# Kernel tuning notes

Hardware: AMD Instinct MI355X
Metric: run time of the kernel (lower is better)

The kernel has to match this reference:

```python
import jax, jax.numpy as jnp
import numpy as np
from jax.scipy.special import logsumexp

SINKHORN_ITERS = 10


def _fix_coupling_sinkhorn(lc, lp1, lp2, iterations=SINKHORN_ITERS):
    # lc: [Z,S], lp1: [Z], lp2: [S]
    for _ in range(iterations):
        lc = lc + lp1[:, None] - logsumexp(lc, axis=1, keepdims=True)
        lc = lc + lp2[None, :] - logsumexp(lc, axis=0, keepdims=True)
    return lc


def _fix_coupling_rejection(lc, lp1, lp2):
    fixed_p1 = lc + lp1[:, None] - logsumexp(lc, axis=1, keepdims=True)
    approx_lp2 = logsumexp(fixed_p1, axis=0)
    accept = lp2 - approx_lp2
    accept = accept - jnp.max(accept)
    acc_s2_given_s1 = jax.nn.log_softmax(fixed_p1, axis=-1) + accept[None, :]
    log_keep = logsumexp(acc_s2_given_s1, axis=-1)
    certainly_keep = jnp.exp(log_keep) >= 1.0
    resample = jnp.where(
        certainly_keep, -jnp.inf,
        jnp.log1p(-jnp.where(certainly_keep, 0.0, jnp.exp(log_keep))))
    compensation = resample[:, None] + lp2[None, :]
    return lp1[:, None] + jnp.logaddexp(acc_s2_given_s1, compensation)


def setup_inputs() -> dict:
    key = jax.random.key(0)
    ks = jax.random.split(key, 8)
    B, S, Z, H1, H2 = 64, 512, 1024, 512, 256
    return {
        "s_logits": jax.random.normal(ks[0], (B, S), jnp.float32),
        "W1": jax.random.normal(ks[1], (S, H1), jnp.float32) / np.sqrt(S),
        "b1": jnp.zeros((H1,), jnp.float32),
        "W2": jax.random.normal(ks[2], (H1, H2), jnp.float32) / np.sqrt(H1),
        "b2": jnp.zeros((H2,), jnp.float32),
        "Wout": jax.random.normal(ks[3], (H2, Z, S), jnp.float32) / np.sqrt(H2),
        "bout": jnp.zeros((Z, S), jnp.float32),
        "prior": jax.random.normal(ks[4], (Z,), jnp.float32) * 0.05,
    }


def reference(s_logits, W1, b1, W2, b2, Wout, bout, prior):
    z_logits = jax.nn.log_softmax(prior)  # [Z]

    def get_joint(sl):  # sl: [S]
        v = jax.nn.softmax(sl)
        v = jax.nn.sigmoid(v @ W1 + b1)
        v = jax.nn.sigmoid(v @ W2 + b2)
        log_joint = jnp.einsum('h,hzs->zs', v, Wout) + bout  # [Z,S]
        log_joint = _fix_coupling_sinkhorn(log_joint, z_logits, sl)
        return _fix_coupling_rejection(log_joint, z_logits, sl)

    return jax.vmap(get_joint)(s_logits)  # [B,Z,S]
```

## Files before the change

### kernel.cpp

```cpp
#include <hip/hip_runtime.h>
#include <math.h>

#define Bn 64
#define Sn 512
#define Zn 1024
#define H1n 512
#define H2n 256
#define ZSn (Zn*Sn)

#define OFF_LP1  0
#define OFF_VT   1024
#define OFF_V    17408
#define OFF_W    50176
#define OFF_R    82944
#define OFF_PM   148480
#define OFF_PS   672768
#define OFF_VB   1200128
#define OFF_KB   1310720
#define NEED_BF16_BYTES ((size_t)OFF_KB*4 + (size_t)Bn*ZSn*2)

#define NINF (-__builtin_inff())

typedef __attribute__((ext_vector_type(8))) short          s16x8;
typedef __attribute__((ext_vector_type(8))) unsigned short u16x8;
typedef __attribute__((ext_vector_type(4))) float          f32x4;

__device__ __forceinline__ float wred_max(float x){
#pragma unroll
  for (int o=32;o;o>>=1) x = fmaxf(x, __shfl_xor(x, o, 64));
  return x;
}
__device__ __forceinline__ float wred_sum(float x){
#pragma unroll
  for (int o=32;o;o>>=1) x += __shfl_xor(x, o, 64);
  return x;
}
__device__ __forceinline__ float lae(float a, float c){
  float m = fmaxf(a,c), n = fminf(a,c);
  return m + log1pf(__expf(n-m));
}
__device__ __forceinline__ float toF(float v){ return v; }
__device__ __forceinline__ float toF(unsigned short v){ return __uint_as_float(((unsigned int)v)<<16); }
__device__ __forceinline__ unsigned short bf16rne(float f){
  unsigned int u = __float_as_uint(f);
  return (unsigned short)((u + 0x7fffu + ((u>>16)&1u)) >> 16);
}
__device__ __forceinline__ unsigned int pack2(float a, float b){
  unsigned int ua = __float_as_uint(a), ub = __float_as_uint(b);
  ua = (ua + 0x7fffu + ((ua>>16)&1u)) >> 16;
  ub = (ub + 0x7fffu + ((ub>>16)&1u)) & 0xffff0000u;
  return ua | ub;
}

__global__ __launch_bounds__(512) void prep_kernel(const float* __restrict__ prior,
                                                   float* __restrict__ ws){
  __shared__ float red[8];
  int t = threadIdx.x;
  float x0 = prior[t], x1 = prior[t+512];
  float m = wred_max(fmaxf(x0,x1));
  if ((t&63)==0) red[t>>6] = m;
  __syncthreads();
  float M = red[0];
#pragma unroll
  for (int i=1;i<8;i++) M = fmaxf(M, red[i]);
  float e = __expf(x0-M)+__expf(x1-M);
  e = wred_sum(e);
  __syncthreads();
  if ((t&63)==0) red[t>>6] = e;
  __syncthreads();
  float T = 0.f;
#pragma unroll
  for (int i=0;i<8;i++) T += red[i];
  float lse = M + logf(T);
  ws[OFF_LP1 + t]       = x0 - lse;
  ws[OFF_LP1 + t + 512] = x1 - lse;
}

__global__ __launch_bounds__(512) void mlp_kernel(const float* __restrict__ sl,
    const float* __restrict__ W1, const float* __restrict__ b1,
    const float* __restrict__ W2, const float* __restrict__ b2,
    float* __restrict__ ws, int wbf){
  __shared__ float p[Sn];
  __shared__ float h1s[H1n];
  __shared__ float red[8];
  int b = blockIdx.x, t = threadIdx.x;
  float x = sl[b*Sn + t];
  float m = wred_max(x);
  if ((t&63)==0) red[t>>6] = m;
  __syncthreads();
  float M = red[0];
#pragma unroll
  for (int i=1;i<8;i++) M = fmaxf(M, red[i]);
  float e = __expf(x-M);
  float es = wred_sum(e);
  __syncthreads();
  if ((t&63)==0) red[t>>6] = es;
  __syncthreads();
  float T = 0.f;
#pragma unroll
  for (int i=0;i<8;i++) T += red[i];
  p[t] = e / T;
  __syncthreads();
  float acc = b1[t];
#pragma unroll 8
  for (int s=0;s<Sn;s++) acc = fmaf(p[s], W1[s*H1n + t], acc);
  h1s[t] = 1.f/(1.f+__expf(-acc));
  __syncthreads();
  if (t < H2n){
    float a2 = b2[t];
#pragma unroll 8
    for (int s=0;s<H1n;s++) a2 = fmaf(h1s[s], W2[s*H2n + t], a2);
    float vv = 1.f/(1.f+__expf(-a2));
    ws[OFF_VT + t*Bn + b] = vv;
    if (wbf) ((unsigned short*)(ws + OFF_VB))[b*H2n + t] = bf16rne(vv);
  }
}

template<int BF>
__global__ __launch_bounds__(256,1) void gemm_kernel(const float* __restrict__ Wout,
    const float* __restrict__ bout, const float* __restrict__ ws,
    float* __restrict__ Kf, unsigned int* __restrict__ Kb){
  int zh = blockIdx.x*256 + threadIdx.x;
  const float* __restrict__ VT = ws + OFF_VT;
  float2 acc[Bn];
#pragma unroll
  for (int b=0;b<Bn;b++){ acc[b].x = 0.f; acc[b].y = 0.f; }
  const float2* Wp = (const float2*)Wout;
#pragma unroll 2
  for (int h=0; h<H2n; h++){
    float2 wv = Wp[(size_t)h*(ZSn/2) + zh];
    const float* vh = VT + (h<<6);
#pragma unroll
    for (int b=0;b<Bn;b++){
      acc[b].x = fmaf(vh[b], wv.x, acc[b].x);
      acc[b].y = fmaf(vh[b], wv.y, acc[b].y);
    }
  }
  float2 bb = ((const float2*)bout)[zh];
#pragma unroll
  for (int b=0;b<Bn;b++){
    float ax = acc[b].x + bb.x, ay = acc[b].y + bb.y;
    if (BF){
      Kb[(size_t)b*(ZSn/2) + zh] = pack2(ax, ay);
    } else {
      float2 o; o.x = ax; o.y = ay;
      ((float2*)Kf)[(size_t)b*(ZSn/2) + zh] = o;
    }
  }
}

__global__ __launch_bounds__(256,3) void gemm_mfma(const float* __restrict__ Wout,
    const float* __restrict__ bout, const float* __restrict__ ws,
    unsigned short* __restrict__ Kb){
  __shared__ unsigned short Vsh[64*264];
  __shared__ float Bsh[32*65];
  int t = threadIdx.x;
  int zs0 = blockIdx.x * 64;

  {
    const unsigned short* vsrc = (const unsigned short*)(ws + OFF_VB);
    int vrow = t >> 2, vq = t & 3;
#pragma unroll
    for (int i=0;i<8;i++)
      *(u16x8*)&Vsh[vrow*264 + vq*64 + i*8] = *(const u16x8*)&vsrc[vrow*256 + vq*64 + i*8];
  }

  int w  = t >> 6;
  int l  = t & 63;
  int q  = l & 15;
  int kg = l >> 4;
  int sh = t >> 3, sf = t & 7;

  float bo = bout[zs0 + (w<<4) + q];

  f32x4 acc[4] = {{0.f,0.f,0.f,0.f},{0.f,0.f,0.f,0.f},{0.f,0.f,0.f,0.f},{0.f,0.f,0.f,0.f}};

  const float4* src = (const float4*)(Wout + (size_t)sh * ZSn + zs0);
  float4 ra = src[sf], rb = src[sf+8];

  for (int ks=0; ks<8; ks++){
    __syncthreads();
    {
      float* drow = &Bsh[sh*65 + (sf<<2)];
      drow[0]=ra.x; drow[1]=ra.y; drow[2]=ra.z; drow[3]=ra.w;
      drow[32]=rb.x; drow[33]=rb.y; drow[34]=rb.z; drow[35]=rb.w;
    }
    if (ks < 7){
      const float4* s2 = (const float4*)(Wout + (size_t)((ks+1)*32 + sh) * ZSn + zs0);
      ra = s2[sf]; rb = s2[sf+8];
    }
    __syncthreads();
    float bf[8];
#pragma unroll
    for (int j=0;j<8;j++) bf[j] = Bsh[(kg*8+j)*65 + (w<<4) + q];
    unsigned int pk[4];
#pragma unroll
    for (int j=0;j<4;j++)
      asm("v_cvt_pk_bf16_f32 %0, %1, %2" : "=v"(pk[j]) : "v"(bf[2*j]), "v"(bf[2*j+1]));
    union { unsigned int u[4]; s16x8 v; } bu;
    bu.u[0]=pk[0]; bu.u[1]=pk[1]; bu.u[2]=pk[2]; bu.u[3]=pk[3];
#pragma unroll
    for (int mt=0; mt<4; mt++){
      s16x8 af = *(const s16x8*)&Vsh[(mt*16 + q)*264 + ks*32 + kg*8];
      acc[mt] = __builtin_amdgcn_mfma_f32_16x16x32_bf16(af, bu.v, acc[mt], 0, 0, 0);
    }
  }
#pragma unroll
  for (int mt=0; mt<4; mt++){
#pragma unroll
    for (int r=0; r<4; r++){
      int b = mt*16 + kg*4 + r;
      Kb[(size_t)b*ZSn + zs0 + (w<<4) + q] = bf16rne(acc[mt][r] + bo);
    }
  }
}

template<typename KT>
__global__ __launch_bounds__(512) void iter_fused(const KT* __restrict__ Kg,
    float* __restrict__ ws, const float* __restrict__ sl, int iter, int mode){
  __shared__ KT Ksh[64*512];
  __shared__ float vsh[512];
  __shared__ float ush[64];
  __shared__ float lsh[64];
  int t = threadIdx.x;
  int b = blockIdx.x >> 4, c = blockIdx.x & 15;
  const float4* s4 = (const float4*)(Kg + ((size_t)((b<<10) + (c<<6)) << 9));
  float4* d4 = (float4*)Ksh;
  constexpr int NV = (int)sizeof(KT)*4;
#pragma unroll
  for (int i=0;i<NV;i++) d4[i*512 + t] = s4[i*512 + t];
  if (t < 64) lsh[t] = ws[OFF_LP1 + (c<<6) + t];
  float v_s;
  if (iter == 0) v_s = 0.f;
  else {
    float M = NINF, S = 0.f;
#pragma unroll
    for (int cc=0; cc<16; cc++){
      float m = ws[OFF_PM + ((b*16+cc)<<9) + t];
      float p = ws[OFF_PS + ((b*16+cc)<<9) + t];
      float nm = fmaxf(M, m);
      S = S*__expf(M-nm) + p*__expf(m-nm);
      M = nm;
    }
    v_s = sl[(b<<9) + t] - (M + logf(S));
  }
  vsh[t] = v_s;
  if (mode) ws[OFF_V + (b<<9) + t] = v_s;
  __syncthreads();
  int l = t & 63, w = t >> 6;
  float vr[8];
#pragma unroll
  for (int j=0;j<8;j++) vr[j] = vsh[(l<<3)+j];
#pragma unroll
  for (int rr=0; rr<8; rr++){
    int row = (w<<3) + rr;
    float x[8];
    if constexpr (sizeof(KT)==2){
      u16x8 kv = *(const u16x8*)&Ksh[(row<<9) + (l<<3)];
#pragma unroll
      for (int j=0;j<8;j++) x[j] = toF((unsigned short)kv[j]) + vr[j];
    } else {
      const float4* kp = (const float4*)&Ksh[(row<<9) + (l<<3)];
      float4 k0 = kp[0], k1 = kp[1];
      x[0]=k0.x+vr[0]; x[1]=k0.y+vr[1]; x[2]=k0.z+vr[2]; x[3]=k0.w+vr[3];
      x[4]=k1.x+vr[4]; x[5]=k1.y+vr[5]; x[6]=k1.z+vr[6]; x[7]=k1.w+vr[7];
    }
    float m = NINF;
#pragma unroll
    for (int j=0;j<8;j++) m = fmaxf(m, x[j]);
    m = wred_max(m);
    float s = 0.f;
#pragma unroll
    for (int j=0;j<8;j++) s += __expf(x[j]-m);
    s = wred_sum(s);
    float L = m + logf(s);
    if (l == 0){
      ush[row] = lsh[row] - L;
      if (mode) ws[OFF_R + (b<<10) + (c<<6) + row] = L;
    }
  }
  __syncthreads();
  float M0 = NINF, S0 = 0.f, M1 = NINF, S1 = 0.f;
#pragma unroll 8
  for (int i=0;i<32;i++){
    float xa = toF(Ksh[(i<<9) + t]) + ush[i];
    float na = fmaxf(M0, xa);
    S0 = S0*__expf(M0-na) + __expf(xa-na);
    M0 = na;
    float xb = toF(Ksh[((i+32)<<9) + t]) + ush[i+32];
    float nb = fmaxf(M1, xb);
    S1 = S1*__expf(M1-nb) + __expf(xb-nb);
    M1 = nb;
  }
  float M = fmaxf(M0, M1);
  float S = S0*__expf(M0-M) + S1*__expf(M1-M);
  ws[OFF_PM + ((b*16+c)<<9) + t] = M;
  ws[OFF_PS + ((b*16+c)<<9) + t] = S;
}

__global__ __launch_bounds__(512) void wker(float* __restrict__ ws, const float* __restrict__ sl){
  __shared__ float red[8];
  int b = blockIdx.x, s = threadIdx.x;
  float M = NINF, S = 0.f;
#pragma unroll
  for (int cc=0; cc<16; cc++){
    float m = ws[OFF_PM + ((b*16+cc)<<9) + s];
    float p = ws[OFF_PS + ((b*16+cc)<<9) + s];
    float nm = fmaxf(M, m);
    S = S*__expf(M-nm) + p*__expf(m-nm);
    M = nm;
  }
  float L = M + logf(S);
  float v = ws[OFF_V + (b<<9) + s];
  float araw = sl[(b<<9)+s] - v - L;
  float mm = wred_max(araw);
  if ((s&63)==0) red[s>>6] = mm;
  __syncthreads();
  float amax = red[0];
#pragma unroll
  for (int i=1;i<8;i++) amax = fmaxf(amax, red[i]);
  ws[OFF_W + (b<<9) + s] = v + araw - amax;
}

template<typename KT>
__global__ __launch_bounds__(512) void final_fused(const KT* __restrict__ Kg,
    float* __restrict__ out, const float* __restrict__ ws, const float* __restrict__ sl){
  int t = threadIdx.x, l = t & 63, wv = t >> 6;
  int row = blockIdx.x*8 + wv;
  int b = row >> 10, z = row & (Zn-1);
  const KT* Kr = Kg + ((size_t)row << 9);
  const float* wr = ws + OFF_W + (b << 9);
  const float* pr = sl + (b << 9);
  float r  = ws[OFF_R + row];
  float l1 = ws[OFF_LP1 + z];
  float ww[8], pp[8], kk[8];
  {
    const float4* wp = (const float4*)(wr + (l<<3));
    float4 w0 = wp[0], w1 = wp[1];
    ww[0]=w0.x; ww[1]=w0.y; ww[2]=w0.z; ww[3]=w0.w;
    ww[4]=w1.x; ww[5]=w1.y; ww[6]=w1.z; ww[7]=w1.w;
    const float4* pt = (const float4*)(pr + (l<<3));
    float4 p0 = pt[0], p1 = pt[1];
    pp[0]=p0.x; pp[1]=p0.y; pp[2]=p0.z; pp[3]=p0.w;
    pp[4]=p1.x; pp[5]=p1.y; pp[6]=p1.z; pp[7]=p1.w;
  }
  if constexpr (sizeof(KT)==2){
    u16x8 kv = *(const u16x8*)&Kr[l<<3];
#pragma unroll
    for (int j=0;j<8;j++) kk[j] = toF((unsigned short)kv[j]);
  } else {
    const float4* kp = (const float4*)&Kr[l<<3];
    float4 k0 = kp[0], k1 = kp[1];
    kk[0]=k0.x; kk[1]=k0.y; kk[2]=k0.z; kk[3]=k0.w;
    kk[4]=k1.x; kk[5]=k1.y; kk[6]=k1.z; kk[7]=k1.w;
  }
  float a[8], m = NINF;
#pragma unroll
  for (int j=0;j<8;j++){
    a[j] = kk[j] - r + ww[j];
    m = fmaxf(m, a[j]);
  }
  m = wred_max(m);
  float s = 0.f;
#pragma unroll
  for (int j=0;j<8;j++) s += __expf(a[j]-m);
  s = wred_sum(s);
  float lk = m + logf(s);
  float rs = (lk >= 0.f) ? NINF : log1pf(-__expf(lk));
  float o[8];
#pragma unroll
  for (int j=0;j<8;j++) o[j] = l1 + lae(a[j], rs + pp[j]);
  float4 o0, o1;
  o0.x=o[0]; o0.y=o[1]; o0.z=o[2]; o0.w=o[3];
  o1.x=o[4]; o1.y=o[5]; o1.z=o[6]; o1.w=o[7];
  float4* op = (float4*)(out + ((size_t)row << 9) + (l<<3));
  op[0] = o0; op[1] = o1;
}

extern "C" void kernel_launch(void* const* d_in, const int* in_sizes, int n_in,
                              void* d_out, int out_size, void* d_ws, size_t ws_size,
                              hipStream_t stream) {
  const float* sl    = (const float*)d_in[0];
  const float* W1    = (const float*)d_in[1];
  const float* b1    = (const float*)d_in[2];
  const float* W2    = (const float*)d_in[3];
  const float* b2    = (const float*)d_in[4];
  const float* Wout  = (const float*)d_in[5];
  const float* bout  = (const float*)d_in[6];
  const float* prior = (const float*)d_in[7];
  float* ws = (float*)d_ws;
  float* Kf = (float*)d_out;
  unsigned short* Kb = (unsigned short*)(ws + OFF_KB);
  const bool use_bf16 = (ws_size >= NEED_BF16_BYTES);

  prep_kernel<<<1, 512, 0, stream>>>(prior, ws);
  mlp_kernel<<<Bn, 512, 0, stream>>>(sl, W1, b1, W2, b2, ws, use_bf16 ? 1 : 0);

  if (use_bf16){
    gemm_mfma<<<ZSn/64, 256, 0, stream>>>(Wout, bout, ws, Kb);
    for (int it = 0; it < 10; ++it)
      iter_fused<unsigned short><<<Bn*16, 512, 0, stream>>>(Kb, ws, sl, it, 0);
    iter_fused<unsigned short><<<Bn*16, 512, 0, stream>>>(Kb, ws, sl, 10, 1);
    wker<<<Bn, 512, 0, stream>>>(ws, sl);
    final_fused<unsigned short><<<Bn*Zn/8, 512, 0, stream>>>(Kb, (float*)d_out, ws, sl);
  } else {
    gemm_kernel<0><<<ZSn/512, 256, 0, stream>>>(Wout, bout, ws, Kf, nullptr);
    for (int it = 0; it < 10; ++it)
      iter_fused<float><<<Bn*16, 512, 0, stream>>>(Kf, ws, sl, it, 0);
    iter_fused<float><<<Bn*16, 512, 0, stream>>>(Kf, ws, sl, 10, 1);
    wker<<<Bn, 512, 0, stream>>>(ws, sl);
    final_fused<float><<<Bn*Zn/8, 512, 0, stream>>>(Kf, (float*)d_out, ws, sl);
  }
}
```

Baseline: 1.326 ms.

## Fuse Sinkhorn iterations and rejection into one register-resident cooperative kernel

Replaces the eleven iter_fused launches, wker and final_fused with a single cooperative kernel. Each block keeps its 256x512 bf16 slice of the coupling in registers across all iterations, synchronises via grid.sync, and exchanges only per-column partial sums through global memory. This removes repeated re-reads of the 64MB bf16 tensor and the per-iteration launch overhead. The cost is very high register pressure (16 uint4 per thread at 1024 threads), possible spills, and a reliance on all 256 blocks being co-resident; if the cooperative launch fails it falls back to the old path.

```diff
diff --git a/kernel.cpp b/kernel.cpp
--- a/kernel.cpp
+++ b/kernel.cpp
@@ -1,5 +1,8 @@
 #include <hip/hip_runtime.h>
+#include <hip/hip_cooperative_groups.h>
 #include <math.h>
+
+namespace cg = cooperative_groups;
 
 #define Bn 64
 #define Sn 512
@@ -15,6 +18,7 @@
 #define OFF_R    82944
 #define OFF_PM   148480
 #define OFF_PS   672768
+#define OFF_C    1197056
 #define OFF_VB   1200128
 #define OFF_KB   1310720
 #define NEED_BF16_BYTES ((size_t)OFF_KB*4 + (size_t)Bn*ZSn*2)
@@ -41,6 +45,8 @@
 }
 __device__ __forceinline__ float toF(float v){ return v; }
 __device__ __forceinline__ float toF(unsigned short v){ return __uint_as_float(((unsigned int)v)<<16); }
+__device__ __forceinline__ float bflo(unsigned int u){ return __uint_as_float(u<<16); }
+__device__ __forceinline__ float bfhi(unsigned int u){ return __uint_as_float(u & 0xffff0000u); }
 __device__ __forceinline__ unsigned short bf16rne(float f){
   unsigned int u = __float_as_uint(f);
   return (unsigned short)((u + 0x7fffu + ((u>>16)&1u)) >> 16);
@@ -99,6 +105,7 @@
   float T = 0.f;
 #pragma unroll
   for (int i=0;i<8;i++) T += red[i];
+  if (t == 0) ws[OFF_C + b] = M + logf(T);
   p[t] = e / T;
   __syncthreads();
   float acc = b1[t];
@@ -212,6 +219,145 @@
       int b = mt*16 + kg*4 + r;
       Kb[(size_t)b*ZSn + zs0 + (w<<4) + q] = bf16rne(acc[mt][r] + bo);
     }
+  }
+}
+
+__global__ __launch_bounds__(1024, 4) void coop_sinkhorn(
+    const unsigned short* __restrict__ Kb, float* __restrict__ ws,
+    const float* __restrict__ sl, float* __restrict__ out){
+  __shared__ float msh[16*512];
+  __shared__ float lsh[256];
+  int t = threadIdx.x;
+  int l = t & 63, w = t >> 6;
+  int blk = blockIdx.x;
+  int b = blk >> 2, zc = blk & 3;
+  int z0 = zc << 8;
+
+  uint4 kreg[16];
+  {
+    const uint4* Kp = (const uint4*)Kb;
+    size_t rbase = ((size_t)((b<<10) + z0 + (w<<4)))*64 + (size_t)l;
+#pragma unroll
+    for (int r=0;r<16;r++) kreg[r] = Kp[rbase + (size_t)r*64];
+  }
+  if (t < 256) lsh[t] = ws[OFF_LP1 + z0 + t];
+
+  float c = ws[OFF_C + b];
+  float prn[8];
+  {
+    const float4* p4 = (const float4*)(sl + (b<<9) + (l<<3));
+    float4 a = p4[0], d = p4[1];
+    prn[0]=a.x-c; prn[1]=a.y-c; prn[2]=a.z-c; prn[3]=a.w-c;
+    prn[4]=d.x-c; prn[5]=d.y-c; prn[6]=d.z-c; prn[7]=d.w-c;
+  }
+  __syncthreads();
+
+  float* pbuf0 = ws + OFF_PM;
+  float* pbuf1 = ws + OFF_PM + 64*512*4;
+  cg::grid_group grid = cg::this_grid();
+
+  float v[8];
+  for (int it=0; it<=10; ++it){
+    if (it == 0){
+#pragma unroll
+      for (int j=0;j<8;j++) v[j]=0.f;
+    } else {
+      const float* pb = (it & 1) ? pbuf0 : pbuf1;
+#pragma unroll
+      for (int j=0;j<8;j++){
+        int s = (l<<3)+j;
+        float4 s4 = *(const float4*)(pb + (((size_t)(b<<9)+s)<<2));
+        float S = (s4.x + s4.y) + (s4.z + s4.w);
+        v[j] = prn[j] - __logf(S);
+      }
+    }
+    float colT[8];
+#pragma unroll
+    for (int j=0;j<8;j++) colT[j]=0.f;
+#pragma unroll
+    for (int r=0;r<16;r++){
+      uint4 kv = kreg[r];
+      float ex[8];
+      ex[0]=__expf(bflo(kv.x)+v[0]); ex[1]=__expf(bfhi(kv.x)+v[1]);
+      ex[2]=__expf(bflo(kv.y)+v[2]); ex[3]=__expf(bfhi(kv.y)+v[3]);
+      ex[4]=__expf(bflo(kv.z)+v[4]); ex[5]=__expf(bfhi(kv.z)+v[5]);
+      ex[6]=__expf(bflo(kv.w)+v[6]); ex[7]=__expf(bfhi(kv.w)+v[7]);
+      float s = 0.f;
+#pragma unroll
+      for (int j=0;j<8;j++) s += ex[j];
+      s = wred_sum(s);
+      float eu = __expf(lsh[(w<<4)+r] - __logf(s));
+#pragma unroll
+      for (int j=0;j<8;j++) colT[j] = fmaf(ex[j], eu, colT[j]);
+    }
+    {
+      float4 c0, c1;
+      c0.x=colT[0]*__expf(-v[0]); c0.y=colT[1]*__expf(-v[1]);
+      c0.z=colT[2]*__expf(-v[2]); c0.w=colT[3]*__expf(-v[3]);
+      c1.x=colT[4]*__expf(-v[4]); c1.y=colT[5]*__expf(-v[5]);
+      c1.z=colT[6]*__expf(-v[6]); c1.w=colT[7]*__expf(-v[7]);
+      float4* d = (float4*)&msh[w*512 + (l<<3)];
+      d[0]=c0; d[1]=c1;
+    }
+    __syncthreads();
+    if (t < 512){
+      float S = 0.f;
+#pragma unroll
+      for (int ww=0; ww<16; ww++) S += msh[ww*512 + t];
+      float* pw = (it & 1) ? pbuf1 : pbuf0;
+      pw[(((size_t)(b<<9)+t)<<2) + zc] = S;
+    }
+    __threadfence();
+    grid.sync();
+  }
+
+  float dj[8], ed[8];
+  {
+    float am = NINF;
+#pragma unroll
+    for (int j=0;j<8;j++){
+      int s = (l<<3)+j;
+      float4 s4 = *(const float4*)(pbuf0 + (((size_t)(b<<9)+s)<<2));
+      float Lc = __logf((s4.x + s4.y) + (s4.z + s4.w));
+      dj[j] = prn[j] - v[j] - Lc;
+      am = fmaxf(am, dj[j]);
+    }
+    am = wred_max(am);
+#pragma unroll
+    for (int j=0;j<8;j++){ dj[j] -= am; ed[j] = __expf(dj[j]); }
+  }
+#pragma unroll
+  for (int r=0;r<16;r++){
+    uint4 kv = kreg[r];
+    float x[8], ex[8];
+    x[0]=bflo(kv.x)+v[0]; x[1]=bfhi(kv.x)+v[1];
+    x[2]=bflo(kv.y)+v[2]; x[3]=bfhi(kv.y)+v[3];
+    x[4]=bflo(kv.z)+v[4]; x[5]=bfhi(kv.z)+v[5];
+    x[6]=bflo(kv.w)+v[6]; x[7]=bfhi(kv.w)+v[7];
+    float s = 0.f, sa = 0.f;
+#pragma unroll
+    for (int j=0;j<8;j++){
+      ex[j] = __expf(x[j]);
+      s  += ex[j];
+      sa += ex[j]*ed[j];
+    }
+    s = wred_sum(s); sa = wred_sum(sa);
+    float L  = __logf(s);
+    float lk = __logf(sa) - L;
+    float rs = (lk >= 0.f) ? NINF : log1pf(-__expf(lk));
+    float l1 = lsh[(w<<4)+r];
+    int z = z0 + (w<<4) + r;
+    float o[8];
+#pragma unroll
+    for (int j=0;j<8;j++){
+      float a = x[j] + dj[j] - L;
+      o[j] = l1 + lae(a, rs + prn[j] + c);
+    }
+    float4 o0, o1;
+    o0.x=o[0]; o0.y=o[1]; o0.z=o[2]; o0.w=o[3];
+    o1.x=o[4]; o1.y=o[5]; o1.z=o[6]; o1.w=o[7];
+    float4* op = (float4*)(out + (((size_t)(b<<10) + z)<<9) + (l<<3));
+    op[0]=o0; op[1]=o1;
   }
 }
 
@@ -398,11 +544,21 @@
 
   if (use_bf16){
     gemm_mfma<<<ZSn/64, 256, 0, stream>>>(Wout, bout, ws, Kb);
-    for (int it = 0; it < 10; ++it)
-      iter_fused<unsigned short><<<Bn*16, 512, 0, stream>>>(Kb, ws, sl, it, 0);
-    iter_fused<unsigned short><<<Bn*16, 512, 0, stream>>>(Kb, ws, sl, 10, 1);
-    wker<<<Bn, 512, 0, stream>>>(ws, sl);
-    final_fused<unsigned short><<<Bn*Zn/8, 512, 0, stream>>>(Kb, (float*)d_out, ws, sl);
+    const unsigned short* KbA = Kb;
+    float* wsA = ws;
+    const float* slA = sl;
+    float* outA = (float*)d_out;
+    void* args[] = { (void*)&KbA, (void*)&wsA, (void*)&slA, (void*)&outA };
+    hipError_t rc = hipLaunchCooperativeKernel((const void*)coop_sinkhorn,
+                                               dim3(256), dim3(1024), args, 0, stream);
+    if (rc != hipSuccess){
+      (void)hipGetLastError();
+      for (int it = 0; it < 10; ++it)
+        iter_fused<unsigned short><<<Bn*16, 512, 0, stream>>>(Kb, ws, sl, it, 0);
+      iter_fused<unsigned short><<<Bn*16, 512, 0, stream>>>(Kb, ws, sl, 10, 1);
+      wker<<<Bn, 512, 0, stream>>>(ws, sl);
+      final_fused<unsigned short><<<Bn*Zn/8, 512, 0, stream>>>(Kb, (float*)d_out, ws, sl);
+    }
   } else {
     gemm_kernel<0><<<ZSn/512, 256, 0, stream>>>(Wout, bout, ws, Kf, nullptr);
     for (int it = 0; it < 10; ++it)
```

Result: slower. 3.908 ms (+194.7%).
